# Kernel tuning notes

Measured on AMD Instinct MI355X. Metric: run time of the kernel, lower is better.

Reference implementation:

```python
import jax, jax.numpy as jnp
import numpy as np

D_K = 128
SCALE = 1.0 / np.sqrt(D_K).astype(np.float32)


def setup_inputs() -> dict:
    key = jax.random.key(0)
    kq, kk, kv = jax.random.split(key, 3)
    B, S, D = 8, 2048, D_K
    Q = jax.random.normal(kq, (B, S, D), dtype=jnp.float32)
    K = jax.random.normal(kk, (B, S, D), dtype=jnp.float32)
    V = jax.random.normal(kv, (B, S, D), dtype=jnp.float32)
    # causal mask: 1 = attend, 0 = block (per docstring semantics)
    mask = jnp.tril(jnp.ones((S, S), dtype=jnp.int32))
    return {"Q": Q, "K": K, "V": V, "mask": mask}


def reference(Q, K, V, mask):
    # scores: (B, S, S)
    scores = jnp.einsum("bqd,bkd->bqk", Q, K) * SCALE
    scores = jnp.where(mask == 0, -jnp.inf, scores)
    attention_weights = jax.nn.softmax(scores, axis=-1)
    output = jnp.einsum("bqk,bkd->bqd", attention_weights, V)
    return (output, attention_weights)
```

## Files before the change

### kernel.cpp

```cpp
#include <hip/hip_runtime.h>
#include <stdint.h>

#define BATCH 8
#define SEQ 2048
#define DH 128
#define QT 32
#define KT 64

static constexpr float SCALE_F = 0.08838834764831843f;

using bf16x8 = __attribute__((ext_vector_type(8))) short;
using f32x4  = __attribute__((ext_vector_type(4))) float;

__device__ inline unsigned short f2bf(float f) {
  unsigned u = __float_as_uint(f);
  u += 0x7fff + ((u >> 16) & 1);
  return (unsigned short)(u >> 16);
}

__device__ inline void gload_lds16(const void* g, void* l) {
  __builtin_amdgcn_global_load_lds(
      (const __attribute__((address_space(1))) void*)g,
      (__attribute__((address_space(3))) void*)l, 16, 0, 0);
}

extern "C" __global__ void __launch_bounds__(256)
convert_qk(const float4* __restrict__ Q, const float4* __restrict__ K,
           ushort4* __restrict__ Qb, ushort4* __restrict__ Kb) {
  int i = blockIdx.x * 256 + threadIdx.x;
  float4 q = Q[i];
  float4 k = K[i];
  ushort4 uq, uk;
  uq.x = f2bf(q.x); uq.y = f2bf(q.y); uq.z = f2bf(q.z); uq.w = f2bf(q.w);
  uk.x = f2bf(k.x); uk.y = f2bf(k.y); uk.z = f2bf(k.z); uk.w = f2bf(k.w);
  Qb[i] = uq;
  int r = i >> 5;
  int byte = (i & 31) * 8;
  int sbyte = byte ^ ((r & 7) << 4);
  Kb[(size_t)r * 32 + (sbyte >> 3)] = uk;
}

extern "C" __global__ void __launch_bounds__(256)
convert_v(const float* __restrict__ V, unsigned short* __restrict__ Vt) {
  __shared__ __align__(16) unsigned short L[DH][72];
  const int b = blockIdx.x >> 5;
  const int st = blockIdx.x & 31;
  const int s0 = st * 64;
  const int tid = threadIdx.x;
  const float* Vb = V + ((size_t)b * SEQ + s0) * DH;
#pragma unroll
  for (int it = 0; it < 8; ++it) {
    int f = (it * 256 + tid) * 4;
    int r = f >> 7, d0 = f & 127;
    float4 v = *(const float4*)(Vb + f);
    L[d0 + 0][r] = f2bf(v.x);
    L[d0 + 1][r] = f2bf(v.y);
    L[d0 + 2][r] = f2bf(v.z);
    L[d0 + 3][r] = f2bf(v.w);
  }
  __syncthreads();
  const int d = tid >> 1, h = tid & 1;
  unsigned short* dstb = Vt + ((size_t)b * DH + d) * SEQ + s0;
  const uint4* src = (const uint4*)&L[d][h * 32];
#pragma unroll
  for (int j = 0; j < 4; ++j) {
    int u = h * 4 + j;
    ((uint4*)dstb)[u ^ (d & 7)] = src[j];
  }
}

__global__ __launch_bounds__(256, 4) void attn_sums(
    const unsigned short* __restrict__ Qbf, const unsigned short* __restrict__ Kbf,
    float* __restrict__ Wg) {
  __shared__ __align__(16) unsigned short Ks[2][KT][128];
  __shared__ float red[4][16];

  const int tid = threadIdx.x;
  const int lane = tid & 63;
  const int w = tid >> 6;
  const int l15 = lane & 15;
  const int quad = lane >> 4;
  const int swz = (l15 & 7) << 4;

  const int b = blockIdx.x & 7;
  const int z = blockIdx.x >> 3;
  const int t = (z < 64) ? (127 - z) : (z - 64);
  const int q0 = t * 16;
  const int ntk = (t >> 2) + 1;

  const unsigned short* Qbb = Qbf + (size_t)b * SEQ * DH;
  const unsigned short* Kbb = Kbf + (size_t)b * SEQ * DH;
  float* Wb = Wg + (size_t)b * SEQ * SEQ;

  auto stageK = [&](int buf, int k0) {
#pragma unroll
    for (int it = 0; it < 4; ++it) {
      const unsigned short* g = Kbb + (size_t)k0 * DH + (it * 256 + tid) * 8;
      unsigned short* l = &Ks[buf][0][0] + (it * 256 + w * 64) * 8;
      gload_lds16(g, l);
    }
  };

  bf16x8 qf[4];
#pragma unroll
  for (int ks = 0; ks < 4; ++ks)
    qf[ks] = *(const bf16x8*)(Qbb + (size_t)(q0 + l15) * DH + ks * 32 + quad * 8);

  stageK(0, 0);
  __syncthreads();

  float rs[4] = {0.f, 0.f, 0.f, 0.f};
  int cur = 0;
  for (int kt = 0; kt < ntk; ++kt) {
    if (kt + 1 < ntk) stageK(cur ^ 1, (kt + 1) * KT);
    f32x4 a0 = {0.f, 0.f, 0.f, 0.f};
#pragma unroll
    for (int ks = 0; ks < 4; ++ks) {
      const int cb = ((ks * 64 + quad * 16) ^ swz) >> 1;
      bf16x8 kb = *(const bf16x8*)(&Ks[cur][0][0] + (w * 16 + l15) * 128 + cb);
      a0 = __builtin_amdgcn_mfma_f32_16x16x32_bf16(qf[ks], kb, a0, 0, 0, 0);
    }
    const int kcol = kt * KT + w * 16 + l15;
#pragma unroll
    for (int r = 0; r < 4; ++r) {
      const int row0 = q0 + quad * 4 + r;
      rs[r] += (kcol <= row0) ? __expf(a0[r] * SCALE_F) : 0.f;
    }
    __syncthreads();
    cur ^= 1;
  }

#pragma unroll
  for (int m = 1; m <= 8; m <<= 1) {
#pragma unroll
    for (int r = 0; r < 4; ++r) rs[r] += __shfl_xor(rs[r], m);
  }
  if (l15 == 0) {
#pragma unroll
    for (int r = 0; r < 4; ++r) red[w][quad * 4 + r] = rs[r];
  }
  __syncthreads();
  if (tid < 16) {
    float s = red[0][tid] + red[1][tid] + red[2][tid] + red[3][tid];
    Wb[(size_t)(q0 + tid) * SEQ + (SEQ - 1)] = 1.f / s;
  }
}

__global__ __launch_bounds__(256, 2) void attn_pv(
    const unsigned short* __restrict__ Qbf, const unsigned short* __restrict__ Kbf,
    const unsigned short* __restrict__ Vtg,
    float* __restrict__ Og, float* __restrict__ Wg) {
  __shared__ __align__(16) unsigned short Ks[2][KT][128];
  __shared__ __align__(16) unsigned short Vs[2][DH][64];
  __shared__ __align__(16) unsigned short Ps[QT][72];
  __shared__ __align__(16) float Psf[QT][68];
  __shared__ float redv[QT];

  const int tid = threadIdx.x;
  const int lane = tid & 63;
  const int w = tid >> 6;
  const int l15 = lane & 15;
  const int quad = lane >> 4;
  const int swz = (l15 & 7) << 4;

  const int b = blockIdx.x & 7;
  const int z = blockIdx.x >> 3;
  const int t = (z < 32) ? (63 - z) : (z - 32);
  const int q0 = t * QT;
  const int ntk = t / 2 + 1;

  const unsigned short* Qbb = Qbf + (size_t)b * SEQ * DH;
  const unsigned short* Kbb = Kbf + (size_t)b * SEQ * DH;
  const unsigned short* Vtb = Vtg + (size_t)b * DH * SEQ;
  float* Ob = Og + (size_t)b * SEQ * DH;
  float* Wb = Wg + (size_t)b * SEQ * SEQ;

  auto stageK = [&](int buf, int k0) {
#pragma unroll
    for (int it = 0; it < 4; ++it) {
      const unsigned short* g = Kbb + (size_t)k0 * DH + (it * 256 + tid) * 8;
      unsigned short* l = &Ks[buf][0][0] + (it * 256 + w * 64) * 8;
      gload_lds16(g, l);
    }
  };
  auto stageV = [&](int buf, int k0) {
#pragma unroll
    for (int it = 0; it < 4; ++it) {
      int f = it * 256 + tid;
      int d = f >> 3, u = f & 7;
      const unsigned short* g = Vtb + (size_t)d * SEQ + k0 + u * 8;
      unsigned short* l = &Vs[buf][0][0] + (it * 256 + w * 64) * 8;
      gload_lds16(g, l);
    }
  };

  if (tid < QT) redv[tid] = Wb[(size_t)(q0 + tid) * SEQ + (SEQ - 1)];
  __syncthreads();
  float inv0[4], inv1[4];
#pragma unroll
  for (int r = 0; r < 4; ++r) {
    inv0[r] = redv[quad * 4 + r];
    inv1[r] = redv[16 + quad * 4 + r];
  }

  {
    const int c0f = ntk * KT;
    const int len = SEQ - c0f;
    if (len > 0) {
      const float4 z4 = {0.f, 0.f, 0.f, 0.f};
      for (int r = 0; r < QT; ++r) {
        float* row = Wb + (size_t)(q0 + r) * SEQ + c0f;
        for (int c = tid * 4; c < len; c += 1024) *(float4*)(row + c) = z4;
      }
    }
  }

  bf16x8 qf0[4], qf1[4];
#pragma unroll
  for (int ks = 0; ks < 4; ++ks) {
    qf0[ks] = *(const bf16x8*)(Qbb + (size_t)(q0 + l15) * DH + ks * 32 + quad * 8);
    qf1[ks] = *(const bf16x8*)(Qbb + (size_t)(q0 + 16 + l15) * DH + ks * 32 + quad * 8);
  }

  stageK(0, 0);
  stageV(0, 0);
  __syncthreads();

  f32x4 o00 = {0.f, 0.f, 0.f, 0.f}, o01 = {0.f, 0.f, 0.f, 0.f};
  f32x4 o10 = {0.f, 0.f, 0.f, 0.f}, o11 = {0.f, 0.f, 0.f, 0.f};
  const int srow = tid >> 3;
  const int sc0 = (tid & 7) * 8;
  int cur = 0;
  for (int kt = 0; kt < ntk; ++kt) {
    if (kt + 1 < ntk) {
      stageK(cur ^ 1, (kt + 1) * KT);
      stageV(cur ^ 1, (kt + 1) * KT);
    }
    f32x4 a0 = {0.f, 0.f, 0.f, 0.f};
    f32x4 a1 = {0.f, 0.f, 0.f, 0.f};
#pragma unroll
    for (int ks = 0; ks < 4; ++ks) {
      const int cb = ((ks * 64 + quad * 16) ^ swz) >> 1;
      bf16x8 kb = *(const bf16x8*)(&Ks[cur][0][0] + (w * 16 + l15) * 128 + cb);
      a0 = __builtin_amdgcn_mfma_f32_16x16x32_bf16(qf0[ks], kb, a0, 0, 0, 0);
      a1 = __builtin_amdgcn_mfma_f32_16x16x32_bf16(qf1[ks], kb, a1, 0, 0, 0);
    }
    const int kcol = kt * KT + w * 16 + l15;
#pragma unroll
    for (int r = 0; r < 4; ++r) {
      const int row0 = q0 + quad * 4 + r;
      const int row1 = row0 + 16;
      float p0 = (kcol <= row0) ? __expf(a0[r] * SCALE_F) * inv0[r] : 0.f;
      float p1 = (kcol <= row1) ? __expf(a1[r] * SCALE_F) * inv1[r] : 0.f;
      Ps[quad * 4 + r][kcol - kt * KT] = f2bf(p0);
      Ps[16 + quad * 4 + r][kcol - kt * KT] = f2bf(p1);
      Psf[quad * 4 + r][kcol - kt * KT] = p0;
      Psf[16 + quad * 4 + r][kcol - kt * KT] = p1;
    }
    __syncthreads();
#pragma unroll
    for (int ks = 0; ks < 2; ++ks) {
      bf16x8 pa0 = *(const bf16x8*)&Ps[l15][ks * 32 + quad * 8];
      bf16x8 pa1 = *(const bf16x8*)&Ps[16 + l15][ks * 32 + quad * 8];
      const int cb = ((ks * 64 + quad * 16) ^ swz) >> 1;
      bf16x8 v0 = *(const bf16x8*)(&Vs[cur][0][0] + (w * 32 + l15) * 64 + cb);
      bf16x8 v1 = *(const bf16x8*)(&Vs[cur][0][0] + (w * 32 + 16 + l15) * 64 + cb);
      o00 = __builtin_amdgcn_mfma_f32_16x16x32_bf16(pa0, v0, o00, 0, 0, 0);
      o01 = __builtin_amdgcn_mfma_f32_16x16x32_bf16(pa0, v1, o01, 0, 0, 0);
      o10 = __builtin_amdgcn_mfma_f32_16x16x32_bf16(pa1, v0, o10, 0, 0, 0);
      o11 = __builtin_amdgcn_mfma_f32_16x16x32_bf16(pa1, v1, o11, 0, 0, 0);
    }
    {
      float4 x0 = *(const float4*)&Psf[srow][sc0];
      float4 x1 = *(const float4*)&Psf[srow][sc0 + 4];
      float* dst = Wb + (size_t)(q0 + srow) * SEQ + kt * KT + sc0;
      *(float4*)dst = x0;
      *(float4*)(dst + 4) = x1;
    }
    __syncthreads();
    cur ^= 1;
  }

#pragma unroll
  for (int r = 0; r < 4; ++r) {
    const int row0 = q0 + quad * 4 + r;
    const int row1 = row0 + 16;
    Ob[(size_t)row0 * DH + w * 32 + l15] = o00[r];
    Ob[(size_t)row0 * DH + w * 32 + 16 + l15] = o01[r];
    Ob[(size_t)row1 * DH + w * 32 + l15] = o10[r];
    Ob[(size_t)row1 * DH + w * 32 + 16 + l15] = o11[r];
  }
}

#define FQT 32
__global__ __launch_bounds__(256, 2) void attn_fb(
    const float* __restrict__ Qg, const float* __restrict__ Kg,
    const float* __restrict__ Vg, float* __restrict__ Og, float* __restrict__ Wg) {
  __shared__ __align__(16) unsigned short Qs[FQT][136];
  __shared__ __align__(16) unsigned short Ks[KT][136];
  __shared__ __align__(16) unsigned short Vs[DH][72];
  __shared__ __align__(16) unsigned short Ps[FQT][72];
  __shared__ float red[4][FQT];

  const int tid = threadIdx.x;
  const int lane = tid & 63;
  const int w = tid >> 6;
  const int l15 = lane & 15;
  const int quad = lane >> 4;

  const int b = blockIdx.x >> 5;
  const int z = blockIdx.x & 31;

  const float* Qgb = Qg + (size_t)b * SEQ * DH;
  const float* Kgb = Kg + (size_t)b * SEQ * DH;
  const float* Vgb = Vg + (size_t)b * SEQ * DH;
  float* Ob = Og + (size_t)b * SEQ * DH;
  float* Wb = Wg + (size_t)b * SEQ * SEQ;

  auto stageK = [&](int k0) {
#pragma unroll
    for (int it = 0; it < 8; ++it) {
      int f = (it * 256 + tid) * 4;
      int r = f >> 7, d0 = f & 127;
      float4 v = *(const float4*)(Kgb + (size_t)(k0 + r) * DH + d0);
      ushort4 u;
      u.x = f2bf(v.x); u.y = f2bf(v.y); u.z = f2bf(v.z); u.w = f2bf(v.w);
      *(ushort4*)&Ks[r][d0] = u;
    }
  };
  auto stageV = [&](int k0) {
#pragma unroll
    for (int it = 0; it < 8; ++it) {
      int f = (it * 256 + tid) * 4;
      int r = f >> 7, d0 = f & 127;
      float4 v = *(const float4*)(Vgb + (size_t)(k0 + r) * DH + d0);
      Vs[d0 + 0][r] = f2bf(v.x);
      Vs[d0 + 1][r] = f2bf(v.y);
      Vs[d0 + 2][r] = f2bf(v.z);
      Vs[d0 + 3][r] = f2bf(v.w);
    }
  };

  const int tiles[2] = {z, 63 - z};
  for (int ti = 0; ti < 2; ++ti) {
    const int t = tiles[ti];
    const int q0 = t * FQT;
    const int ntk = t / 2 + 1;
    {
      const int c0f = ntk * KT;
      const int len = SEQ - c0f;
      if (len > 0) {
        const float4 z4 = {0.f, 0.f, 0.f, 0.f};
        for (int r = 0; r < FQT; ++r) {
          float* row = Wb + (size_t)(q0 + r) * SEQ + c0f;
          for (int c = tid * 4; c < len; c += 1024) *(float4*)(row + c) = z4;
        }
      }
    }
    __syncthreads();
#pragma unroll
    for (int it = 0; it < 4; ++it) {
      int f = (it * 256 + tid) * 4;
      int r = f >> 7, d0 = f & 127;
      float4 v = *(const float4*)(Qgb + (size_t)(q0 + r) * DH + d0);
      ushort4 u;
      u.x = f2bf(v.x); u.y = f2bf(v.y); u.z = f2bf(v.z); u.w = f2bf(v.w);
      *(ushort4*)&Qs[r][d0] = u;
    }
    float rs0[4] = {0.f, 0.f, 0.f, 0.f};
    float rs1[4] = {0.f, 0.f, 0.f, 0.f};
    for (int kt = 0; kt < ntk; ++kt) {
      __syncthreads();
      stageK(kt * KT);
      __syncthreads();
      f32x4 a0 = {0.f, 0.f, 0.f, 0.f};
      f32x4 a1 = {0.f, 0.f, 0.f, 0.f};
#pragma unroll
      for (int ks = 0; ks < 4; ++ks) {
        bf16x8 qa0 = *(const bf16x8*)&Qs[l15][ks * 32 + quad * 8];
        bf16x8 qa1 = *(const bf16x8*)&Qs[16 + l15][ks * 32 + quad * 8];
        bf16x8 kb = *(const bf16x8*)&Ks[w * 16 + l15][ks * 32 + quad * 8];
        a0 = __builtin_amdgcn_mfma_f32_16x16x32_bf16(qa0, kb, a0, 0, 0, 0);
        a1 = __builtin_amdgcn_mfma_f32_16x16x32_bf16(qa1, kb, a1, 0, 0, 0);
      }
      const int kcol = kt * KT + w * 16 + l15;
#pragma unroll
      for (int r = 0; r < 4; ++r) {
        const int row0 = q0 + quad * 4 + r;
        const int row1 = row0 + 16;
        rs0[r] += (kcol <= row0) ? __expf(a0[r] * SCALE_F) : 0.f;
        rs1[r] += (kcol <= row1) ? __expf(a1[r] * SCALE_F) : 0.f;
      }
    }
#pragma unroll
    for (int m = 1; m <= 8; m <<= 1) {
#pragma unroll
      for (int r = 0; r < 4; ++r) {
        rs0[r] += __shfl_xor(rs0[r], m);
        rs1[r] += __shfl_xor(rs1[r], m);
      }
    }
    __syncthreads();
    if (l15 == 0) {
#pragma unroll
      for (int r = 0; r < 4; ++r) {
        red[w][quad * 4 + r] = rs0[r];
        red[w][16 + quad * 4 + r] = rs1[r];
      }
    }
    __syncthreads();
    float inv0[4], inv1[4];
#pragma unroll
    for (int r = 0; r < 4; ++r) {
      float s0 = red[0][quad * 4 + r] + red[1][quad * 4 + r] +
                 red[2][quad * 4 + r] + red[3][quad * 4 + r];
      float s1 = red[0][16 + quad * 4 + r] + red[1][16 + quad * 4 + r] +
                 red[2][16 + quad * 4 + r] + red[3][16 + quad * 4 + r];
      inv0[r] = 1.f / s0;
      inv1[r] = 1.f / s1;
    }
    f32x4 o00 = {0.f, 0.f, 0.f, 0.f}, o01 = {0.f, 0.f, 0.f, 0.f};
    f32x4 o10 = {0.f, 0.f, 0.f, 0.f}, o11 = {0.f, 0.f, 0.f, 0.f};
    for (int kt = 0; kt < ntk; ++kt) {
      __syncthreads();
      stageK(kt * KT);
      stageV(kt * KT);
      __syncthreads();
      f32x4 a0 = {0.f, 0.f, 0.f, 0.f};
      f32x4 a1 = {0.f, 0.f, 0.f, 0.f};
#pragma unroll
      for (int ks = 0; ks < 4; ++ks) {
        bf16x8 qa0 = *(const bf16x8*)&Qs[l15][ks * 32 + quad * 8];
        bf16x8 qa1 = *(const bf16x8*)&Qs[16 + l15][ks * 32 + quad * 8];
        bf16x8 kb = *(const bf16x8*)&Ks[w * 16 + l15][ks * 32 + quad * 8];
        a0 = __builtin_amdgcn_mfma_f32_16x16x32_bf16(qa0, kb, a0, 0, 0, 0);
        a1 = __builtin_amdgcn_mfma_f32_16x16x32_bf16(qa1, kb, a1, 0, 0, 0);
      }
      const int kcol = kt * KT + w * 16 + l15;
#pragma unroll
      for (int r = 0; r < 4; ++r) {
        const int row0 = q0 + quad * 4 + r;
        const int row1 = row0 + 16;
        float p0 = (kcol <= row0) ? __expf(a0[r] * SCALE_F) * inv0[r] : 0.f;
        float p1 = (kcol <= row1) ? __expf(a1[r] * SCALE_F) * inv1[r] : 0.f;
        Wb[(size_t)row0 * SEQ + kcol] = p0;
        Wb[(size_t)row1 * SEQ + kcol] = p1;
        Ps[quad * 4 + r][w * 16 + l15] = f2bf(p0);
        Ps[16 + quad * 4 + r][w * 16 + l15] = f2bf(p1);
      }
      __syncthreads();
#pragma unroll
      for (int ks = 0; ks < 2; ++ks) {
        bf16x8 pa0 = *(const bf16x8*)&Ps[l15][ks * 32 + quad * 8];
        bf16x8 pa1 = *(const bf16x8*)&Ps[16 + l15][ks * 32 + quad * 8];
        bf16x8 v0 = *(const bf16x8*)&Vs[w * 32 + l15][ks * 32 + quad * 8];
        bf16x8 v1 = *(const bf16x8*)&Vs[w * 32 + 16 + l15][ks * 32 + quad * 8];
        o00 = __builtin_amdgcn_mfma_f32_16x16x32_bf16(pa0, v0, o00, 0, 0, 0);
        o01 = __builtin_amdgcn_mfma_f32_16x16x32_bf16(pa0, v1, o01, 0, 0, 0);
        o10 = __builtin_amdgcn_mfma_f32_16x16x32_bf16(pa1, v0, o10, 0, 0, 0);
        o11 = __builtin_amdgcn_mfma_f32_16x16x32_bf16(pa1, v1, o11, 0, 0, 0);
      }
    }
#pragma unroll
    for (int r = 0; r < 4; ++r) {
      const int row0 = q0 + quad * 4 + r;
      const int row1 = row0 + 16;
      Ob[(size_t)row0 * DH + w * 32 + l15] = o00[r];
      Ob[(size_t)row0 * DH + w * 32 + 16 + l15] = o01[r];
      Ob[(size_t)row1 * DH + w * 32 + l15] = o10[r];
      Ob[(size_t)row1 * DH + w * 32 + 16 + l15] = o11[r];
    }
  }
}

extern "C" void kernel_launch(void* const* d_in, const int* in_sizes, int n_in,
                              void* d_out, int out_size, void* d_ws, size_t ws_size,
                              hipStream_t stream) {
  const float* Q = (const float*)d_in[0];
  const float* K = (const float*)d_in[1];
  const float* V = (const float*)d_in[2];
  float* Out = (float*)d_out;
  float* W = Out + (size_t)BATCH * SEQ * DH;

  const size_t nel = (size_t)BATCH * SEQ * DH;
  const size_t need = nel * 2 * 3;
  if (ws_size >= need) {
    unsigned short* Qbf = (unsigned short*)d_ws;
    unsigned short* Kbf = Qbf + nel;
    unsigned short* Vt = Kbf + nel;
    hipLaunchKernelGGL(convert_qk, dim3((unsigned)(nel / 4 / 256)), dim3(256), 0, stream,
                       (const float4*)Q, (const float4*)K, (ushort4*)Qbf, (ushort4*)Kbf);
    hipLaunchKernelGGL(convert_v, dim3(BATCH * (SEQ / 64)), dim3(256), 0, stream, V, Vt);
    hipLaunchKernelGGL(attn_sums, dim3(BATCH * 128), dim3(256), 0, stream,
                       Qbf, Kbf, W);
    hipLaunchKernelGGL(attn_pv, dim3(BATCH * 64), dim3(256), 0, stream,
                       Qbf, Kbf, Vt, Out, W);
  } else {
    hipLaunchKernelGGL(attn_fb, dim3(BATCH * 32), dim3(256), 0, stream,
                       Q, K, V, Out, W);
  }
}
```

Baseline: 220.0 us.

## Halve attn_pv query tile to 16 rows and single-buffer V

```diff
diff --git a/kernel.cpp b/kernel.cpp
--- a/kernel.cpp
+++ b/kernel.cpp
@@ -146,15 +146,14 @@
   }
 }
 
-__global__ __launch_bounds__(256, 2) void attn_pv(
+__global__ __launch_bounds__(256, 3) void attn_pv(
     const unsigned short* __restrict__ Qbf, const unsigned short* __restrict__ Kbf,
     const unsigned short* __restrict__ Vtg,
     float* __restrict__ Og, float* __restrict__ Wg) {
   __shared__ __align__(16) unsigned short Ks[2][KT][128];
-  __shared__ __align__(16) unsigned short Vs[2][DH][64];
-  __shared__ __align__(16) unsigned short Ps[QT][72];
-  __shared__ __align__(16) float Psf[QT][68];
-  __shared__ float redv[QT];
+  __shared__ __align__(16) unsigned short Vs[DH][64];
+  __shared__ __align__(16) unsigned short Ps[16][72];
+  __shared__ float redv[16];
 
   const int tid = threadIdx.x;
   const int lane = tid & 63;
@@ -165,9 +164,9 @@
 
   const int b = blockIdx.x & 7;
   const int z = blockIdx.x >> 3;
-  const int t = (z < 32) ? (63 - z) : (z - 32);
-  const int q0 = t * QT;
-  const int ntk = t / 2 + 1;
+  const int t = (z < 64) ? (127 - z) : (z - 64);
+  const int q0 = t * 16;
+  const int ntk = (t >> 2) + 1;
 
   const unsigned short* Qbb = Qbf + (size_t)b * SEQ * DH;
   const unsigned short* Kbb = Kbf + (size_t)b * SEQ * DH;
@@ -183,112 +182,84 @@
       gload_lds16(g, l);
     }
   };
-  auto stageV = [&](int buf, int k0) {
+  auto stageV = [&](int k0) {
 #pragma unroll
     for (int it = 0; it < 4; ++it) {
       int f = it * 256 + tid;
       int d = f >> 3, u = f & 7;
       const unsigned short* g = Vtb + (size_t)d * SEQ + k0 + u * 8;
-      unsigned short* l = &Vs[buf][0][0] + (it * 256 + w * 64) * 8;
+      unsigned short* l = &Vs[0][0] + (it * 256 + w * 64) * 8;
       gload_lds16(g, l);
     }
   };
 
-  if (tid < QT) redv[tid] = Wb[(size_t)(q0 + tid) * SEQ + (SEQ - 1)];
+  if (tid < 16) redv[tid] = Wb[(size_t)(q0 + tid) * SEQ + (SEQ - 1)];
   __syncthreads();
-  float inv0[4], inv1[4];
-#pragma unroll
-  for (int r = 0; r < 4; ++r) {
-    inv0[r] = redv[quad * 4 + r];
-    inv1[r] = redv[16 + quad * 4 + r];
-  }
+  float inv0[4];
+#pragma unroll
+  for (int r = 0; r < 4; ++r) inv0[r] = redv[quad * 4 + r];
 
   {
     const int c0f = ntk * KT;
     const int len = SEQ - c0f;
     if (len > 0) {
       const float4 z4 = {0.f, 0.f, 0.f, 0.f};
-      for (int r = 0; r < QT; ++r) {
+      for (int r = 0; r < 16; ++r) {
         float* row = Wb + (size_t)(q0 + r) * SEQ + c0f;
         for (int c = tid * 4; c < len; c += 1024) *(float4*)(row + c) = z4;
       }
     }
   }
 
-  bf16x8 qf0[4], qf1[4];
-#pragma unroll
-  for (int ks = 0; ks < 4; ++ks) {
-    qf0[ks] = *(const bf16x8*)(Qbb + (size_t)(q0 + l15) * DH + ks * 32 + quad * 8);
-    qf1[ks] = *(const bf16x8*)(Qbb + (size_t)(q0 + 16 + l15) * DH + ks * 32 + quad * 8);
-  }
+  bf16x8 qf[4];
+#pragma unroll
+  for (int ks = 0; ks < 4; ++ks)
+    qf[ks] = *(const bf16x8*)(Qbb + (size_t)(q0 + l15) * DH + ks * 32 + quad * 8);
 
   stageK(0, 0);
-  stageV(0, 0);
+  stageV(0);
   __syncthreads();
 
   f32x4 o00 = {0.f, 0.f, 0.f, 0.f}, o01 = {0.f, 0.f, 0.f, 0.f};
-  f32x4 o10 = {0.f, 0.f, 0.f, 0.f}, o11 = {0.f, 0.f, 0.f, 0.f};
-  const int srow = tid >> 3;
-  const int sc0 = (tid & 7) * 8;
   int cur = 0;
   for (int kt = 0; kt < ntk; ++kt) {
-    if (kt + 1 < ntk) {
-      stageK(cur ^ 1, (kt + 1) * KT);
-      stageV(cur ^ 1, (kt + 1) * KT);
-    }
+    const bool nxt = (kt + 1) < ntk;
+    if (nxt) stageK(cur ^ 1, (kt + 1) * KT);
     f32x4 a0 = {0.f, 0.f, 0.f, 0.f};
-    f32x4 a1 = {0.f, 0.f, 0.f, 0.f};
 #pragma unroll
     for (int ks = 0; ks < 4; ++ks) {
       const int cb = ((ks * 64 + quad * 16) ^ swz) >> 1;
       bf16x8 kb = *(const bf16x8*)(&Ks[cur][0][0] + (w * 16 + l15) * 128 + cb);
-      a0 = __builtin_amdgcn_mfma_f32_16x16x32_bf16(qf0[ks], kb, a0, 0, 0, 0);
-      a1 = __builtin_amdgcn_mfma_f32_16x16x32_bf16(qf1[ks], kb, a1, 0, 0, 0);
+      a0 = __builtin_amdgcn_mfma_f32_16x16x32_bf16(qf[ks], kb, a0, 0, 0, 0);
     }
     const int kcol = kt * KT + w * 16 + l15;
 #pragma unroll
     for (int r = 0; r < 4; ++r) {
       const int row0 = q0 + quad * 4 + r;
-      const int row1 = row0 + 16;
       float p0 = (kcol <= row0) ? __expf(a0[r] * SCALE_F) * inv0[r] : 0.f;
-      float p1 = (kcol <= row1) ? __expf(a1[r] * SCALE_F) * inv1[r] : 0.f;
-      Ps[quad * 4 + r][kcol - kt * KT] = f2bf(p0);
-      Ps[16 + quad * 4 + r][kcol - kt * KT] = f2bf(p1);
-      Psf[quad * 4 + r][kcol - kt * KT] = p0;
-      Psf[16 + quad * 4 + r][kcol - kt * KT] = p1;
+      Wb[(size_t)row0 * SEQ + kcol] = p0;
+      Ps[quad * 4 + r][w * 16 + l15] = f2bf(p0);
     }
     __syncthreads();
 #pragma unroll
     for (int ks = 0; ks < 2; ++ks) {
       bf16x8 pa0 = *(const bf16x8*)&Ps[l15][ks * 32 + quad * 8];
-      bf16x8 pa1 = *(const bf16x8*)&Ps[16 + l15][ks * 32 + quad * 8];
       const int cb = ((ks * 64 + quad * 16) ^ swz) >> 1;
-      bf16x8 v0 = *(const bf16x8*)(&Vs[cur][0][0] + (w * 32 + l15) * 64 + cb);
-      bf16x8 v1 = *(const bf16x8*)(&Vs[cur][0][0] + (w * 32 + 16 + l15) * 64 + cb);
+      bf16x8 v0 = *(const bf16x8*)(&Vs[0][0] + (w * 32 + l15) * 64 + cb);
+      bf16x8 v1 = *(const bf16x8*)(&Vs[0][0] + (w * 32 + 16 + l15) * 64 + cb);
       o00 = __builtin_amdgcn_mfma_f32_16x16x32_bf16(pa0, v0, o00, 0, 0, 0);
       o01 = __builtin_amdgcn_mfma_f32_16x16x32_bf16(pa0, v1, o01, 0, 0, 0);
-      o10 = __builtin_amdgcn_mfma_f32_16x16x32_bf16(pa1, v0, o10, 0, 0, 0);
-      o11 = __builtin_amdgcn_mfma_f32_16x16x32_bf16(pa1, v1, o11, 0, 0, 0);
-    }
-    {
-      float4 x0 = *(const float4*)&Psf[srow][sc0];
-      float4 x1 = *(const float4*)&Psf[srow][sc0 + 4];
-      float* dst = Wb + (size_t)(q0 + srow) * SEQ + kt * KT + sc0;
-      *(float4*)dst = x0;
-      *(float4*)(dst + 4) = x1;
-    }
-    __syncthreads();
+    }
+    __syncthreads();
+    if (nxt) stageV((kt + 1) * KT);
     cur ^= 1;
   }
 
 #pragma unroll
   for (int r = 0; r < 4; ++r) {
     const int row0 = q0 + quad * 4 + r;
-    const int row1 = row0 + 16;
     Ob[(size_t)row0 * DH + w * 32 + l15] = o00[r];
     Ob[(size_t)row0 * DH + w * 32 + 16 + l15] = o01[r];
-    Ob[(size_t)row1 * DH + w * 32 + l15] = o10[r];
-    Ob[(size_t)row1 * DH + w * 32 + 16 + l15] = o11[r];
   }
 }
 
@@ -493,7 +464,7 @@
     hipLaunchKernelGGL(convert_v, dim3(BATCH * (SEQ / 64)), dim3(256), 0, stream, V, Vt);
     hipLaunchKernelGGL(attn_sums, dim3(BATCH * 128), dim3(256), 0, stream,
                        Qbf, Kbf, W);
-    hipLaunchKernelGGL(attn_pv, dim3(BATCH * 64), dim3(256), 0, stream,
+    hipLaunchKernelGGL(attn_pv, dim3(BATCH * 128), dim3(256), 0, stream,
                        Qbf, Kbf, Vt, Out, W);
   } else {
     hipLaunchKernelGGL(attn_fb, dim3(BATCH * 32), dim3(256), 0, stream,
```

New measurement: 215.7 us. No clear change (-1.9%).
